# Performance work log

Hardware: AMD Instinct MI355X
Metric: run time of the kernel (lower is better)

Reference implementation:

```python
import jax, jax.numpy as jnp
import numpy as np

N = 8192
D = 200


def setup_inputs() -> dict:
    key = jax.random.key(0)
    k1, k2, k3 = jax.random.split(key, 3)
    G_p = jax.random.normal(k1, (N, D), dtype=jnp.float32)
    # scale weights so exp(b + e) stays in a sane numeric range
    wb = jax.random.normal(k2, (D, 1), dtype=jnp.float32) * 0.02
    we = jax.random.normal(k3, (D, 1), dtype=jnp.float32) * 0.02
    return {"G_p": G_p, "wb": wb, "we": we, "k": 100}


def reference(G_p, wb, we, k):
    # begin / end scores: [N, 1]
    b_P = G_p @ wb
    e_P = G_p @ we
    # outer-sum span scores -> [N, N]
    numerator = jnp.exp(b_P + e_P.T)
    denominator = jnp.sum(numerator)
    candidate_probs = numerator / denominator
    upper = jnp.triu(candidate_probs)
    flat = upper.reshape(-1)
    k_max_values, flat_idx = jax.lax.top_k(flat, k)
    W = upper.shape[1]
    orig_indices = jnp.stack([flat_idx // W, flat_idx % W], axis=1)
    return orig_indices, k_max_values
```

## Files before the change

### kernel.cpp

```cpp
#include <hip/hip_runtime.h>
#include <math.h>

#define NN 8192
#define DD 200
#define KK 100

#define NBINS 1024
#define HSCALE 64.0f
#define BINW 0.015625f
#define CAND_CAP 4096
#define ROW_CAP 1024
#define COL_CAP 1024

#define OFF_B 0
#define OFF_E 8192

__global__ __launch_bounds__(256) void k_be(const float* __restrict__ G,
                                            const float* __restrict__ wb,
                                            const float* __restrict__ we,
                                            float* __restrict__ wsf) {
    int gid = blockIdx.x * 256 + threadIdx.x;
    int row = gid >> 6;
    int lane = gid & 63;
    float pb = 0.f, pe = 0.f;
    if (lane < 50) {
        float4 g = ((const float4*)(G + (size_t)row * DD))[lane];
        float4 B = ((const float4*)wb)[lane];
        float4 E = ((const float4*)we)[lane];
        pb = fmaf(g.x, B.x, fmaf(g.y, B.y, fmaf(g.z, B.z, g.w * B.w)));
        pe = fmaf(g.x, E.x, fmaf(g.y, E.y, fmaf(g.z, E.z, g.w * E.w)));
    }
    for (int off = 32; off; off >>= 1) {
        pb += __shfl_xor(pb, off, 64);
        pe += __shfl_xor(pe, off, 64);
    }
    if (lane == 0) { wsf[OFF_B + row] = pb; wsf[OFF_E + row] = pe; }
}

__global__ __launch_bounds__(1024) void k_tail(const float* __restrict__ wsf,
                                               float* __restrict__ out) {
    __shared__ float    b_s[NN];
    __shared__ float    e_s[NN];
    __shared__ float    cv[CAND_CAP];
    __shared__ unsigned ci[CAND_CAP];
    __shared__ unsigned sfx[NBINS];
    __shared__ unsigned hbl[NBINS];
    __shared__ int      rows_s[ROW_CAP];
    __shared__ float    rowb_s[ROW_CAP];
    __shared__ int      cols_s[COL_CAP];
    __shared__ float    cole_s[COL_CAP];
    __shared__ float    fr_sb[16], fr_se[16], fr_em[16], fr_bm[16];
    __shared__ unsigned wred[16], wtail_s[16];
    __shared__ unsigned nrows_s, ncols_s, ncand_s;
    __shared__ int      lo_s;
    __shared__ float    sums_s[4];

    int tid = threadIdx.x, wave = tid >> 6, lane = tid & 63;

    sfx[tid] = 0u; hbl[tid] = 0u;
    if (tid == 0) { nrows_s = 0u; ncols_s = 0u; ncand_s = 0u; lo_s = 0; }
    __syncthreads();

    float leb = 0.f, lee = 0.f, lem = -1e30f, lbm = -1e30f;
    const float4* b4 = (const float4*)(wsf + OFF_B);
    const float4* e4 = (const float4*)(wsf + OFF_E);
    for (int i = tid; i < NN / 4; i += 1024) {
        float4 bv = b4[i], ev = e4[i];
        ((float4*)b_s)[i] = bv;
        ((float4*)e_s)[i] = ev;
        leb += expf(bv.x) + expf(bv.y) + expf(bv.z) + expf(bv.w);
        lee += expf(ev.x) + expf(ev.y) + expf(ev.z) + expf(ev.w);
        lbm = fmaxf(lbm, fmaxf(fmaxf(bv.x, bv.y), fmaxf(bv.z, bv.w)));
        lem = fmaxf(lem, fmaxf(fmaxf(ev.x, ev.y), fmaxf(ev.z, ev.w)));
        int p;
        p = (int)fmaf(bv.x, HSCALE, 512.f); atomicAdd(&hbl[min(max(p,0),NBINS-1)], 1u);
        p = (int)fmaf(bv.y, HSCALE, 512.f); atomicAdd(&hbl[min(max(p,0),NBINS-1)], 1u);
        p = (int)fmaf(bv.z, HSCALE, 512.f); atomicAdd(&hbl[min(max(p,0),NBINS-1)], 1u);
        p = (int)fmaf(bv.w, HSCALE, 512.f); atomicAdd(&hbl[min(max(p,0),NBINS-1)], 1u);
        p = (int)fmaf(ev.x, HSCALE, 512.f); atomicAdd(&sfx[min(max(p,0),NBINS-1)], 1u);
        p = (int)fmaf(ev.y, HSCALE, 512.f); atomicAdd(&sfx[min(max(p,0),NBINS-1)], 1u);
        p = (int)fmaf(ev.z, HSCALE, 512.f); atomicAdd(&sfx[min(max(p,0),NBINS-1)], 1u);
        p = (int)fmaf(ev.w, HSCALE, 512.f); atomicAdd(&sfx[min(max(p,0),NBINS-1)], 1u);
    }
    for (int off = 32; off; off >>= 1) {
        leb += __shfl_xor(leb, off, 64);
        lee += __shfl_xor(lee, off, 64);
        lem = fmaxf(lem, __shfl_xor(lem, off, 64));
        lbm = fmaxf(lbm, __shfl_xor(lbm, off, 64));
    }
    if (lane == 0) { fr_sb[wave] = leb; fr_se[wave] = lee; fr_em[wave] = lem; fr_bm[wave] = lbm; }
    __syncthreads();
    if (tid == 0) {
        float a = 0.f, b = 0.f, c = -1e30f, d = -1e30f;
        for (int i = 0; i < 16; ++i) {
            a += fr_sb[i]; b += fr_se[i];
            c = fmaxf(c, fr_em[i]); d = fmaxf(d, fr_bm[i]);
        }
        sums_s[0] = a; sums_s[1] = b; sums_s[2] = c; sums_s[3] = d;
    }

    unsigned v = sfx[tid];
    for (int off = 1; off < 64; off <<= 1) {
        unsigned t = __shfl_down(v, off, 64);
        if (lane + off < 64) v += t;
    }
    if (lane == 0) wtail_s[wave] = v;
    __syncthreads();
    if (tid == 0) {
        unsigned acc = 0, tails[16];
        for (int w = 15; w >= 0; --w) { tails[w] = acc; acc += wtail_s[w]; }
        for (int w = 0; w < 16; ++w) wtail_s[w] = tails[w];
    }
    __syncthreads();
    sfx[tid] = v + wtail_s[wave];
    __syncthreads();

    const unsigned TARGET = 2u * KK;
    int chunk = 64;
    for (int round = 0; round < 2; ++round) {
        int t = lo_s + (wave + 1) * chunk;
        unsigned c = 0;
        for (int k = 0; k < 16; ++k) {
            int p = lane + (k << 6);
            int idx = t + 512 - p;
            unsigned sv = (idx <= 0) ? sfx[0] : ((idx > NBINS - 1) ? 0u : sfx[idx]);
            c += hbl[p] * sv;
        }
        for (int off = 32; off; off >>= 1) c += __shfl_xor(c, off, 64);
        if (lane == 0) wred[wave] = c;
        __syncthreads();
        if (tid == 0) {
            for (int w = 15; w >= 0; --w)
                if (wred[w] >= TARGET) { lo_s += (w + 1) * chunk; break; }
        }
        __syncthreads();
        chunk >>= 4;
    }
    {
        int t = lo_s + wave + 1;
        if (wave < 3) {
            unsigned c = 0;
            for (int k = 0; k < 16; ++k) {
                int p = lane + (k << 6);
                int idx = t + 512 - p;
                unsigned sv = (idx <= 0) ? sfx[0] : ((idx > NBINS - 1) ? 0u : sfx[idx]);
                c += hbl[p] * sv;
            }
            for (int off = 32; off; off >>= 1) c += __shfl_xor(c, off, 64);
            if (lane == 0) wred[wave] = c;
        }
        __syncthreads();
        if (tid == 0) {
            for (int w = 2; w >= 0; --w)
                if (wred[w] >= TARGET) { lo_s += w + 1; break; }
        }
        __syncthreads();
    }
    float thr = -8.0f + (float)(lo_s - 1) * BINW;
    float emax = sums_s[2], bmax = sums_s[3];

    for (int i = tid; i < NN; i += 1024) {
        float bv = b_s[i];
        if (bv + emax >= thr) {
            unsigned pos = atomicAdd(&nrows_s, 1u);
            if (pos < ROW_CAP) { rows_s[pos] = i; rowb_s[pos] = bv; }
        }
        float ev = e_s[i];
        if (ev + bmax >= thr) {
            unsigned pos = atomicAdd(&ncols_s, 1u);
            if (pos < COL_CAP) { cols_s[pos] = i; cole_s[pos] = ev; }
        }
    }
    __syncthreads();
    int nr = (int)min(nrows_s, (unsigned)ROW_CAP);
    int nc = (int)min(ncols_s, (unsigned)COL_CAP);

    int tot = nr * nc;
    for (int idx = tid; idx < tot; idx += 1024) {
        int ri = idx / nc, cj = idx - ri * nc;
        int r = rows_s[ri], j = cols_s[cj];
        if (j < r) continue;
        float s = rowb_s[ri] + cole_s[cj];
        if (s >= thr) {
            unsigned pos = atomicAdd(&ncand_s, 1u);
            if (pos < CAND_CAP) {
                cv[pos] = s;
                ci[pos] = ((unsigned)r << 13) | (unsigned)j;
            }
        }
    }
    __syncthreads();

    unsigned M = min(ncand_s, (unsigned)CAND_CAP);
    float inv_den = 1.0f / (sums_s[0] * sums_s[1]);
    for (unsigned c2 = tid; c2 < M; c2 += 1024) {
        float vv = cv[c2];
        unsigned fi = ci[c2];
        int rank = 0;
        for (unsigned m = 0; m < M; ++m) {
            float vm = cv[m];
            rank += (vm > vv) || (vm == vv && ci[m] < fi);
        }
        if (rank < KK) {
            out[2 * rank]     = (float)(fi >> 13);
            out[2 * rank + 1] = (float)(fi & 8191u);
            out[200 + rank]   = expf(vv) * inv_den;
        }
    }
}

extern "C" void kernel_launch(void* const* d_in, const int* in_sizes, int n_in,
                              void* d_out, int out_size, void* d_ws, size_t ws_size,
                              hipStream_t stream) {
    const float* G  = (const float*)d_in[0];
    const float* wb = (const float*)d_in[1];
    const float* we = (const float*)d_in[2];
    float* out = (float*)d_out;
    float* wsf = (float*)d_ws;

    hipLaunchKernelGGL(k_be, dim3(2048), dim3(256), 0, stream, G, wb, we, wsf);
    hipLaunchKernelGGL(k_tail, dim3(1), dim3(1024), 0, stream, wsf, out);
}
```

Baseline: 78.07 us.

## Move histogram and exp-sum computation into the parallel projection kernel

The begin/end histograms and per-block partial exp sums are now computed in the grid-wide k_be kernel, using global atomics on a device histogram and per-block partials in the workspace. The single-block tail kernel then only reads and reduces these values and resets the histogram for the next call. This removes serial exp and shared-atomic work from the one-block kernel. In exchange, the exact row and column maxima are replaced by bin upper bounds, which makes the pruning filter looser, and the design relies on a persistent global histogram being zeroed between calls.

```diff
diff --git a/kernel.cpp b/kernel.cpp
--- a/kernel.cpp
+++ b/kernel.cpp
@@ -14,14 +14,20 @@
 
 #define OFF_B 0
 #define OFF_E 8192
+#define OFF_PB 16384
+#define OFF_PE 18432
+
+__device__ unsigned g_hist[2 * NBINS];
 
 __global__ __launch_bounds__(256) void k_be(const float* __restrict__ G,
                                             const float* __restrict__ wb,
                                             const float* __restrict__ we,
                                             float* __restrict__ wsf) {
+    __shared__ float seb[4], see[4];
     int gid = blockIdx.x * 256 + threadIdx.x;
     int row = gid >> 6;
     int lane = gid & 63;
+    int wave = threadIdx.x >> 6;
     float pb = 0.f, pe = 0.f;
     if (lane < 50) {
         float4 g = ((const float4*)(G + (size_t)row * DD))[lane];
@@ -34,7 +40,21 @@
         pb += __shfl_xor(pb, off, 64);
         pe += __shfl_xor(pe, off, 64);
     }
-    if (lane == 0) { wsf[OFF_B + row] = pb; wsf[OFF_E + row] = pe; }
+    if (lane == 0) {
+        wsf[OFF_B + row] = pb;
+        wsf[OFF_E + row] = pe;
+        int p = (int)fmaf(pb, HSCALE, 512.f);
+        atomicAdd(&g_hist[min(max(p, 0), NBINS - 1)], 1u);
+        int q = (int)fmaf(pe, HSCALE, 512.f);
+        atomicAdd(&g_hist[NBINS + min(max(q, 0), NBINS - 1)], 1u);
+        seb[wave] = expf(pb);
+        see[wave] = expf(pe);
+    }
+    __syncthreads();
+    if (threadIdx.x == 0) {
+        wsf[OFF_PB + blockIdx.x] = (seb[0] + seb[1]) + (seb[2] + seb[3]);
+        wsf[OFF_PE + blockIdx.x] = (see[0] + see[1]) + (see[2] + see[3]);
+    }
 }
 
 __global__ __launch_bounds__(1024) void k_tail(const float* __restrict__ wsf,
@@ -49,57 +69,53 @@
     __shared__ float    rowb_s[ROW_CAP];
     __shared__ int      cols_s[COL_CAP];
     __shared__ float    cole_s[COL_CAP];
-    __shared__ float    fr_sb[16], fr_se[16], fr_em[16], fr_bm[16];
+    __shared__ float    fr_sb[16], fr_se[16];
+    __shared__ int      fr_eb[16], fr_bb[16];
     __shared__ unsigned wred[16], wtail_s[16];
     __shared__ unsigned nrows_s, ncols_s, ncand_s;
     __shared__ int      lo_s;
     __shared__ float    sums_s[4];
 
     int tid = threadIdx.x, wave = tid >> 6, lane = tid & 63;
-
-    sfx[tid] = 0u; hbl[tid] = 0u;
     if (tid == 0) { nrows_s = 0u; ncols_s = 0u; ncand_s = 0u; lo_s = 0; }
-    __syncthreads();
-
-    float leb = 0.f, lee = 0.f, lem = -1e30f, lbm = -1e30f;
+
     const float4* b4 = (const float4*)(wsf + OFF_B);
     const float4* e4 = (const float4*)(wsf + OFF_E);
     for (int i = tid; i < NN / 4; i += 1024) {
-        float4 bv = b4[i], ev = e4[i];
-        ((float4*)b_s)[i] = bv;
-        ((float4*)e_s)[i] = ev;
-        leb += expf(bv.x) + expf(bv.y) + expf(bv.z) + expf(bv.w);
-        lee += expf(ev.x) + expf(ev.y) + expf(ev.z) + expf(ev.w);
-        lbm = fmaxf(lbm, fmaxf(fmaxf(bv.x, bv.y), fmaxf(bv.z, bv.w)));
-        lem = fmaxf(lem, fmaxf(fmaxf(ev.x, ev.y), fmaxf(ev.z, ev.w)));
-        int p;
-        p = (int)fmaf(bv.x, HSCALE, 512.f); atomicAdd(&hbl[min(max(p,0),NBINS-1)], 1u);
-        p = (int)fmaf(bv.y, HSCALE, 512.f); atomicAdd(&hbl[min(max(p,0),NBINS-1)], 1u);
-        p = (int)fmaf(bv.z, HSCALE, 512.f); atomicAdd(&hbl[min(max(p,0),NBINS-1)], 1u);
-        p = (int)fmaf(bv.w, HSCALE, 512.f); atomicAdd(&hbl[min(max(p,0),NBINS-1)], 1u);
-        p = (int)fmaf(ev.x, HSCALE, 512.f); atomicAdd(&sfx[min(max(p,0),NBINS-1)], 1u);
-        p = (int)fmaf(ev.y, HSCALE, 512.f); atomicAdd(&sfx[min(max(p,0),NBINS-1)], 1u);
-        p = (int)fmaf(ev.z, HSCALE, 512.f); atomicAdd(&sfx[min(max(p,0),NBINS-1)], 1u);
-        p = (int)fmaf(ev.w, HSCALE, 512.f); atomicAdd(&sfx[min(max(p,0),NBINS-1)], 1u);
-    }
+        ((float4*)b_s)[i] = b4[i];
+        ((float4*)e_s)[i] = e4[i];
+    }
+
+    unsigned hb = g_hist[tid];
+    unsigned he = g_hist[NBINS + tid];
+    g_hist[tid] = 0u;
+    g_hist[NBINS + tid] = 0u;
+    hbl[tid] = hb;
+
+    float psb = wsf[OFF_PB + tid] + wsf[OFF_PB + 1024 + tid];
+    float pse = wsf[OFF_PE + tid] + wsf[OFF_PE + 1024 + tid];
+    int ebin = (he != 0u) ? tid : -1;
+    int bbin = (hb != 0u) ? tid : -1;
     for (int off = 32; off; off >>= 1) {
-        leb += __shfl_xor(leb, off, 64);
-        lee += __shfl_xor(lee, off, 64);
-        lem = fmaxf(lem, __shfl_xor(lem, off, 64));
-        lbm = fmaxf(lbm, __shfl_xor(lbm, off, 64));
-    }
-    if (lane == 0) { fr_sb[wave] = leb; fr_se[wave] = lee; fr_em[wave] = lem; fr_bm[wave] = lbm; }
+        psb += __shfl_xor(psb, off, 64);
+        pse += __shfl_xor(pse, off, 64);
+        ebin = max(ebin, __shfl_xor(ebin, off, 64));
+        bbin = max(bbin, __shfl_xor(bbin, off, 64));
+    }
+    if (lane == 0) { fr_sb[wave] = psb; fr_se[wave] = pse; fr_eb[wave] = ebin; fr_bb[wave] = bbin; }
     __syncthreads();
     if (tid == 0) {
-        float a = 0.f, b = 0.f, c = -1e30f, d = -1e30f;
+        float a = 0.f, b = 0.f; int c = -1, d = -1;
         for (int i = 0; i < 16; ++i) {
             a += fr_sb[i]; b += fr_se[i];
-            c = fmaxf(c, fr_em[i]); d = fmaxf(d, fr_bm[i]);
-        }
-        sums_s[0] = a; sums_s[1] = b; sums_s[2] = c; sums_s[3] = d;
-    }
-
-    unsigned v = sfx[tid];
+            c = max(c, fr_eb[i]); d = max(d, fr_bb[i]);
+        }
+        sums_s[0] = a; sums_s[1] = b;
+        sums_s[2] = -8.0f + (float)(c + 1) * BINW;
+        sums_s[3] = -8.0f + (float)(d + 1) * BINW;
+    }
+
+    unsigned v = he;
     for (int off = 1; off < 64; off <<= 1) {
         unsigned t = __shfl_down(v, off, 64);
         if (lane + off < 64) v += t;
```

After: 110.8 us. 1.42x slower.
